# Kernel tuning notes

Measured on AMD Instinct MI355X. Metric: run time of the kernel, lower is better.

The kernel has to match this reference:

```python
import jax, jax.numpy as jnp
import numpy as np
from jax import lax

B, CIN, H, W = 64, 16, 256, 256
COUT, K = 64, 3

def setup_inputs() -> dict:
    key = jax.random.key(0)
    k1, k2, k3 = jax.random.split(key, 3)
    x = jax.random.normal(k1, (B, CIN, H, W), dtype=jnp.float32)
    # PyTorch Conv2d default init scale ~ 1/sqrt(fan_in)
    fan_in = CIN * K * K
    conv_weight = jax.random.normal(k2, (COUT, CIN, K, K), dtype=jnp.float32) / np.sqrt(fan_in)
    conv_bias = jax.random.normal(k3, (COUT,), dtype=jnp.float32) / np.sqrt(fan_in)
    return {"x": x, "conv_weight": conv_weight, "conv_bias": conv_bias}

def reference(x, conv_weight, conv_bias):
    # conv2d, stride=1, padding=0 (VALID), dilation=1, groups=1
    y = lax.conv_general_dilated(
        x, conv_weight,
        window_strides=(1, 1), padding="VALID",
        dimension_numbers=("NCHW", "OIHW", "NCHW"))
    y = y + conv_bias[None, :, None, None]
    # min over channel dim, keepdim
    y = jnp.min(y, axis=1, keepdims=True)  # [B,1,H',W']
    # double tanh
    return jnp.tanh(jnp.tanh(y))
```

## Files before the change

kernel.cpp:

```cpp
#include <hip/hip_runtime.h>
#include <hip/hip_bf16.h>

#define BATCH 64
#define CIN   16
#define H     256
#define W     256
#define HW    (H*W)
#define COUT  64
#define HO    254
#define WO    254

#define TS     16
#define TIN    18
#define CELL   24
#define NTY    8
#define NITEMS (4*TIN*TIN)
#define IPT    6

typedef short  bf16x8 __attribute__((ext_vector_type(8)));
typedef float  f32x16 __attribute__((ext_vector_type(16)));

static __device__ __forceinline__ unsigned short bfbits(float f) {
    __hip_bfloat16 h = __float2bfloat16(f);
    return *(unsigned short*)&h;
}

static __device__ __forceinline__ bf16x8 ld_frag(const ushort* p) {
    union { uint4 u; bf16x8 b; } cv;
    cv.u = *(const uint4*)p;
    return cv.b;
}

static __device__ __forceinline__ float fast_tanh(float x) {
    x = fminf(fmaxf(x, -15.f), 15.f);
    float e = __expf(2.f * x);
    return (e - 1.f) * __builtin_amdgcn_rcpf(e + 1.f);
}

__global__ void repack_w(const float* __restrict__ w, const float* __restrict__ bias,
                         ushort* __restrict__ wpk) {
    int i = blockIdx.x * 256 + threadIdx.x;
    if (i < 9 * COUT * CIN) {
        int ci   = i & 15;
        int cout = (i >> 4) & 63;
        int tap  = i >> 10;
        wpk[i] = bfbits(w[(cout * CIN + ci) * 9 + tap]);
    } else if (i < 10 * COUT * CIN) {
        int j    = i - 9 * COUT * CIN;
        int ci   = j & 15;
        int cout = j >> 4;
        wpk[i] = (ci == 0) ? bfbits(bias[cout]) : (ushort)0;
    }
}

__global__ __launch_bounds__(256, 2)
void conv_min_tanh_strip(const float* __restrict__ x,
                         const ushort* __restrict__ wpk,
                         float* __restrict__ out) {
    __shared__ __align__(16) ushort xsm[2][TIN * TIN * CELL];

    const int bid = blockIdx.x;
    const int L   = (bid & 7) * 256 + (bid >> 3);
    const int b   = L >> 5;
    const int rr  = L & 31;
    const int yb0 = (rr >> 4) * (NTY * TS);
    const int x0  = (rr & 15) * TS;

    const int tid  = threadIdx.x;
    const int lane = tid & 63;
    const int wv   = tid >> 6;
    const int l31  = lane & 31;
    const int hi   = lane >> 5;

    const float* xp0 = x + (size_t)b * (CIN * HW);
    const float* xp1 = xp0 + HW;
    const float* xp2 = xp0 + 2 * HW;
    const float* xp3 = xp0 + 3 * HW;

    bf16x8 wf[10][2];
    #pragma unroll
    for (int tap = 0; tap < 10; ++tap)
        #pragma unroll
        for (int m = 0; m < 2; ++m)
            wf[tap][m] = ld_frag(wpk + tap * 1024 + (m * 32 + l31) * 16 + hi * 8);

    bf16x8 pone;
    #pragma unroll
    for (int j = 0; j < 8; ++j) pone[j] = 0;
    if (hi == 0) pone[0] = (short)0x3F80;

    int c0[IPT], dyv[IPT], lo[IPT];
    #pragma unroll
    for (int k = 0; k < IPT; ++k) {
        int it = tid + k * 256;
        int dx = it % TIN;
        int t2 = it / TIN;
        int dy = t2 % TIN;
        int cg = t2 / TIN;
        c0[k]  = cg * 4 * HW + min(x0 + dx, W - 1);
        dyv[k] = dy;
        lo[k]  = (dy * TIN + dx) * CELL + cg * 4;
    }

    const int py_b = wv * 4 + (l31 >> 4);
    const int pxc  = l31 & 15;
    const int cb0  = ((py_b + 0) * TIN + pxc) * CELL + hi * 8;
    const int cb1  = ((py_b + 2) * TIN + pxc) * CELL + hi * 8;

    float fxA[IPT][4], fxB[IPT][4];

    auto stage_load = [&](int ybase, float (&fx)[IPT][4]) {
        #pragma unroll
        for (int k = 0; k < IPT; ++k) {
            if (k < 5 || tid < NITEMS - 5 * 256) {
                int gy  = min(ybase + dyv[k], H - 1);
                int idx = c0[k] + (gy << 8);
                fx[k][0] = xp0[idx];
                fx[k][1] = xp1[idx];
                fx[k][2] = xp2[idx];
                fx[k][3] = xp3[idx];
            }
        }
    };
    auto stage_write = [&](int buf, float (&fx)[IPT][4]) {
        #pragma unroll
        for (int k = 0; k < IPT; ++k) {
            if (k < 5 || tid < NITEMS - 5 * 256) {
                ushort4 v;
                v.x = bfbits(fx[k][0]);
                v.y = bfbits(fx[k][1]);
                v.z = bfbits(fx[k][2]);
                v.w = bfbits(fx[k][3]);
                *(ushort4*)&xsm[buf][lo[k]] = v;
            }
        }
    };

    auto tile_barrier = [&]() {
        asm volatile("s_waitcnt lgkmcnt(0)" ::: "memory");
        __builtin_amdgcn_s_barrier();
        asm volatile("" ::: "memory");
    };

    stage_load(yb0, fxA);
    stage_write(0, fxA);
    stage_load(yb0 + TS, fxA);
    tile_barrier();

    auto tile_body = [&](int t, float (&fxw)[IPT][4], float (&fxl)[IPT][4]) {
        const int cur = t & 1;

        if (t + 2 < NTY) stage_load(yb0 + (t + 2) * TS, fxl);

        f32x16 acc[2][2];
        #pragma unroll
        for (int m = 0; m < 2; ++m)
            #pragma unroll
            for (int r = 0; r < 16; ++r) { acc[m][0][r] = 0.f; acc[m][1][r] = 0.f; }

        const ushort* xt = &xsm[cur][0];
        __builtin_amdgcn_s_setprio(1);
        #pragma unroll
        for (int tap = 0; tap < 9; ++tap) {
            const int kh = tap / 3, kw = tap - 3 * kh;
            const int toff = (kh * TIN + kw) * CELL;
            bf16x8 p0 = ld_frag(xt + cb0 + toff);
            bf16x8 p1 = ld_frag(xt + cb1 + toff);
            acc[0][0] = __builtin_amdgcn_mfma_f32_32x32x16_bf16(wf[tap][0], p0, acc[0][0], 0, 0, 0);
            acc[0][1] = __builtin_amdgcn_mfma_f32_32x32x16_bf16(wf[tap][0], p1, acc[0][1], 0, 0, 0);
            acc[1][0] = __builtin_amdgcn_mfma_f32_32x32x16_bf16(wf[tap][1], p0, acc[1][0], 0, 0, 0);
            acc[1][1] = __builtin_amdgcn_mfma_f32_32x32x16_bf16(wf[tap][1], p1, acc[1][1], 0, 0, 0);
        }
        acc[0][0] = __builtin_amdgcn_mfma_f32_32x32x16_bf16(wf[9][0], pone, acc[0][0], 0, 0, 0);
        acc[0][1] = __builtin_amdgcn_mfma_f32_32x32x16_bf16(wf[9][0], pone, acc[0][1], 0, 0, 0);
        acc[1][0] = __builtin_amdgcn_mfma_f32_32x32x16_bf16(wf[9][1], pone, acc[1][0], 0, 0, 0);
        acc[1][1] = __builtin_amdgcn_mfma_f32_32x32x16_bf16(wf[9][1], pone, acc[1][1], 0, 0, 0);
        __builtin_amdgcn_s_setprio(0);

        if (t + 1 < NTY) stage_write(cur ^ 1, fxw);

        float res[2];
        #pragma unroll
        for (int n = 0; n < 2; ++n) {
            float v[16];
            #pragma unroll
            for (int r = 0; r < 16; ++r)
                v[r] = fminf(acc[0][n][r], acc[1][n][r]);
            #pragma unroll
            for (int s = 8; s >= 1; s >>= 1)
                #pragma unroll
                for (int r = 0; r < s; ++r)
                    v[r] = fminf(v[r], v[r + s]);
            res[n] = fminf(v[0], __shfl_xor(v[0], 32, 64));
        }
        float val = hi ? res[1] : res[0];
        int px_lin = wv * 64 + lane;
        int oy = yb0 + t * TS + (px_lin >> 4);
        int ox = x0 + (px_lin & 15);
        if (oy < HO && ox < WO)
            out[((size_t)b * HO + oy) * WO + ox] = fast_tanh(fast_tanh(val));

        tile_barrier();
    };

    #pragma unroll 1
    for (int t = 0; t < NTY; t += 2) {
        tile_body(t,     fxA, fxB);
        tile_body(t + 1, fxB, fxA);
    }
}

extern "C" void kernel_launch(void* const* d_in, const int* in_sizes, int n_in,
                              void* d_out, int out_size, void* d_ws, size_t ws_size,
                              hipStream_t stream) {
    const float* x    = (const float*)d_in[0];
    const float* w    = (const float*)d_in[1];
    const float* bias = (const float*)d_in[2];
    float* out        = (float*)d_out;
    ushort* wpk       = (ushort*)d_ws;

    hipLaunchKernelGGL(repack_w, dim3(40), dim3(256), 0, stream, w, bias, wpk);
    hipLaunchKernelGGL(conv_min_tanh_strip, dim3(2048), dim3(256), 0, stream,
                       x, wpk, out);
}
```

Measured before the change: 108.0 us.

## Give each wave a private LDS slab strip and drop block barriers

Restructures the conv kernel so each of the four waves processes its own 32-row vertical strip in steps of four output rows, staging a private double-buffered 6-row LDS slab. Block-wide barriers between tiles are removed, since each wave only reads data it wrote itself. In exchange, the halo-to-output ratio grows, so each wave loads and converts more redundant input rows per output, and LDS footprint rises.

```diff
diff --git a/kernel.cpp b/kernel.cpp
--- a/kernel.cpp
+++ b/kernel.cpp
@@ -10,12 +10,14 @@
 #define HO    254
 #define WO    254
 
-#define TS     16
-#define TIN    18
-#define CELL   24
-#define NTY    8
-#define NITEMS (4*TIN*TIN)
-#define IPT    6
+#define TS    16
+#define TIN   18
+#define CELL  24
+#define ROWS  6
+#define NB    8
+#define NIT   (4*ROWS*TIN)
+#define IPT   7
+#define SLAB  (ROWS*TIN*CELL)
 
 typedef short  bf16x8 __attribute__((ext_vector_type(8)));
 typedef float  f32x16 __attribute__((ext_vector_type(16)));
@@ -54,16 +56,16 @@
 }
 
 __global__ __launch_bounds__(256, 2)
-void conv_min_tanh_strip(const float* __restrict__ x,
-                         const ushort* __restrict__ wpk,
-                         float* __restrict__ out) {
-    __shared__ __align__(16) ushort xsm[2][TIN * TIN * CELL];
+void conv_min_tanh_wave(const float* __restrict__ x,
+                        const ushort* __restrict__ wpk,
+                        float* __restrict__ out) {
+    __shared__ __align__(16) ushort xsm[4][2][SLAB];
 
     const int bid = blockIdx.x;
     const int L   = (bid & 7) * 256 + (bid >> 3);
     const int b   = L >> 5;
     const int rr  = L & 31;
-    const int yb0 = (rr >> 4) * (NTY * TS);
+    const int yb0 = (rr >> 4) * 128;
     const int x0  = (rr & 15) * TS;
 
     const int tid  = threadIdx.x;
@@ -72,6 +74,8 @@
     const int l31  = lane & 31;
     const int hi   = lane >> 5;
 
+    const int wy0 = yb0 + wv * 32;
+
     const float* xp0 = x + (size_t)b * (CIN * HW);
     const float* xp1 = xp0 + HW;
     const float* xp2 = xp0 + 2 * HW;
@@ -92,27 +96,25 @@
     int c0[IPT], dyv[IPT], lo[IPT];
     #pragma unroll
     for (int k = 0; k < IPT; ++k) {
-        int it = tid + k * 256;
-        int dx = it % TIN;
-        int t2 = it / TIN;
-        int dy = t2 % TIN;
-        int cg = t2 / TIN;
+        int it = lane + k * 64;
+        int cg = it / (ROWS * TIN);
+        int r2 = it - cg * (ROWS * TIN);
+        int dy = r2 / TIN;
+        int dx = r2 - dy * TIN;
         c0[k]  = cg * 4 * HW + min(x0 + dx, W - 1);
         dyv[k] = dy;
         lo[k]  = (dy * TIN + dx) * CELL + cg * 4;
     }
 
-    const int py_b = wv * 4 + (l31 >> 4);
-    const int pxc  = l31 & 15;
-    const int cb0  = ((py_b + 0) * TIN + pxc) * CELL + hi * 8;
-    const int cb1  = ((py_b + 2) * TIN + pxc) * CELL + hi * 8;
-
-    float fxA[IPT][4], fxB[IPT][4];
-
-    auto stage_load = [&](int ybase, float (&fx)[IPT][4]) {
+    const int cb0 = ((l31 >> 4) * TIN + (l31 & 15)) * CELL + hi * 8;
+    const int cb1 = cb0 + 2 * TIN * CELL;
+
+    float fx[IPT][4];
+
+    auto stage_load = [&](int ybase) {
         #pragma unroll
         for (int k = 0; k < IPT; ++k) {
-            if (k < 5 || tid < NITEMS - 5 * 256) {
+            if (k < IPT - 1 || lane < NIT - (IPT - 1) * 64) {
                 int gy  = min(ybase + dyv[k], H - 1);
                 int idx = c0[k] + (gy << 8);
                 fx[k][0] = xp0[idx];
@@ -122,35 +124,27 @@
             }
         }
     };
-    auto stage_write = [&](int buf, float (&fx)[IPT][4]) {
+    auto stage_write = [&](int buf) {
+        ushort* sl = &xsm[wv][buf][0];
         #pragma unroll
         for (int k = 0; k < IPT; ++k) {
-            if (k < 5 || tid < NITEMS - 5 * 256) {
+            if (k < IPT - 1 || lane < NIT - (IPT - 1) * 64) {
                 ushort4 v;
                 v.x = bfbits(fx[k][0]);
                 v.y = bfbits(fx[k][1]);
                 v.z = bfbits(fx[k][2]);
                 v.w = bfbits(fx[k][3]);
-                *(ushort4*)&xsm[buf][lo[k]] = v;
+                *(ushort4*)&sl[lo[k]] = v;
             }
         }
     };
 
-    auto tile_barrier = [&]() {
-        asm volatile("s_waitcnt lgkmcnt(0)" ::: "memory");
-        __builtin_amdgcn_s_barrier();
-        asm volatile("" ::: "memory");
-    };
-
-    stage_load(yb0, fxA);
-    stage_write(0, fxA);
-    stage_load(yb0 + TS, fxA);
-    tile_barrier();
-
-    auto tile_body = [&](int t, float (&fxw)[IPT][4], float (&fxl)[IPT][4]) {
-        const int cur = t & 1;
-
-        if (t + 2 < NTY) stage_load(yb0 + (t + 2) * TS, fxl);
+    stage_load(wy0);
+    stage_write(0);
+
+    #pragma unroll 1
+    for (int t = 0; t < NB; ++t) {
+        if (t + 1 < NB) stage_load(wy0 + (t + 1) * 4);
 
         f32x16 acc[2][2];
         #pragma unroll
@@ -158,7 +152,7 @@
             #pragma unroll
             for (int r = 0; r < 16; ++r) { acc[m][0][r] = 0.f; acc[m][1][r] = 0.f; }
 
-        const ushort* xt = &xsm[cur][0];
+        const ushort* xt = &xsm[wv][t & 1][0];
         __builtin_amdgcn_s_setprio(1);
         #pragma unroll
         for (int tap = 0; tap < 9; ++tap) {
@@ -177,7 +171,7 @@
         acc[1][1] = __builtin_amdgcn_mfma_f32_32x32x16_bf16(wf[9][1], pone, acc[1][1], 0, 0, 0);
         __builtin_amdgcn_s_setprio(0);
 
-        if (t + 1 < NTY) stage_write(cur ^ 1, fxw);
+        if (t + 1 < NB) stage_write((t + 1) & 1);
 
         float res[2];
         #pragma unroll
@@ -194,19 +188,10 @@
             res[n] = fminf(v[0], __shfl_xor(v[0], 32, 64));
         }
         float val = hi ? res[1] : res[0];
-        int px_lin = wv * 64 + lane;
-        int oy = yb0 + t * TS + (px_lin >> 4);
-        int ox = x0 + (px_lin & 15);
+        int oy = wy0 + t * 4 + (lane >> 4);
+        int ox = x0 + (lane & 15);
         if (oy < HO && ox < WO)
             out[((size_t)b * HO + oy) * WO + ox] = fast_tanh(fast_tanh(val));
-
-        tile_barrier();
-    };
-
-    #pragma unroll 1
-    for (int t = 0; t < NTY; t += 2) {
-        tile_body(t,     fxA, fxB);
-        tile_body(t + 1, fxB, fxA);
     }
 }
 
@@ -220,6 +205,6 @@
     ushort* wpk       = (ushort*)d_ws;
 
     hipLaunchKernelGGL(repack_w, dim3(40), dim3(256), 0, stream, w, bias, wpk);
-    hipLaunchKernelGGL(conv_min_tanh_strip, dim3(2048), dim3(256), 0, stream,
+    hipLaunchKernelGGL(conv_min_tanh_wave, dim3(2048), dim3(256), 0, stream,
                        x, wpk, out);
 }
```

Measured after the change: 112.4 us. +4.1%, slower.
